# Kernel tuning notes

Measured on AMD Instinct MI355X. Metric: run time of the kernel, lower is better.

## Reference

```python
import jax, jax.numpy as jnp
import numpy as np

MAX_CLUSTERS = 5
CLUSTER_SIZE_MAX = 3
K_HOP = 2
TAU = 1.0  # epoch=0 -> tau_init * decay^0 = 1.0
NEG = -1e9


def _logits(x, ctx, W1, b1, W2, b2):
    # x: [B,N,D], ctx: [B,H] -> logits [B,N] (selection_mlp, dropout=eval/identity)
    B, N, _ = x.shape
    h = jnp.concatenate([x, jnp.broadcast_to(ctx[:, None, :], (B, N, ctx.shape[-1]))], axis=-1)
    h = jax.nn.relu(h @ W1.T + b1)
    return (h @ W2.T + b2)[..., 0]


def _select(logits, cand, key):
    # Hard Gumbel-Softmax argmax over candidate nodes; zeros row if no candidates.
    any_c = cand.any(axis=-1, keepdims=True)
    ml = jnp.where(cand, logits, NEG)
    u = jax.random.uniform(key, logits.shape, dtype=logits.dtype)
    g = -jnp.log(-jnp.log(u + 1e-8) + 1e-8)
    idx = jnp.argmax((ml + g) / TAU, axis=-1)
    oh = jax.nn.one_hot(idx, logits.shape[-1], dtype=logits.dtype)
    return oh * any_c.astype(logits.dtype)


def _gru(seq, h0, Wih, Whh, bih, bhh):
    # torch nn.GRU single layer, batch_first; seq: [B,T,D], h0: [B,H] -> final hidden [B,H]
    def cell(h, xt):
        gi = xt @ Wih.T + bih
        gh = h @ Whh.T + bhh
        ir, iz, inn = jnp.split(gi, 3, axis=-1)
        hr, hz, hn = jnp.split(gh, 3, axis=-1)
        r = jax.nn.sigmoid(ir + hr)
        z = jax.nn.sigmoid(iz + hz)
        n = jnp.tanh(inn + r * hn)
        return (1.0 - z) * n + z * h, None
    h, _ = jax.lax.scan(cell, h0, jnp.swapaxes(seq, 0, 1))
    return h


def reference(x, adj, mask, W1, b1, W2, b2, Wc, bc, Wih, Whh, bih, bhh):
    B, N, D = x.shape
    key = jax.random.key(42)
    avail = mask.astype(bool)
    ctx = x.mean(axis=1) @ Wc.T + bc          # context_init  [B,H]
    h_gru = jnp.zeros_like(ctx)               # context_hidden
    assign = jnp.zeros((B, N, MAX_CLUSTERS), x.dtype)
    embs, hist = [], []
    for c in range(MAX_CLUSTERS):
        # logits are identical for every selection within this cluster (same x, same context)
        logits = _logits(x, ctx, W1, b1, W2, b2)  # [B,N]
        # seed selection (torch uses .item() -> selection is a constant index; no grad path)
        seed = jax.lax.stop_gradient(_select(logits, avail, jax.random.fold_in(key, 2 * c)))
        avail = avail & ~(seed > 0.5)
        # k-hop BFS from seed via adjacency matvecs
        reach = seed > 0.5
        cur = seed
        for _ in range(K_HOP):
            nb = jnp.einsum('bn,bnm->bm', cur, adj) > 0
            new = nb & ~reach
            reach = reach | nb
            cur = new.astype(x.dtype)
        member = seed
        for a in range(CLUSTER_SIZE_MAX - 1):
            cand = avail & reach
            sel = jax.lax.stop_gradient(_select(logits, cand, jax.random.fold_in(key, 2 * c + 1000 + a)))
            avail = avail & ~(sel > 0.5)
            member = member + sel
        assign = assign.at[:, :, c].set(member)
        cnt = member.sum(axis=-1, keepdims=True)
        emb = jnp.einsum('bn,bnd->bd', member, x) / jnp.maximum(cnt, 1.0)  # mean of member feats; 0 if empty
        embs.append(emb)
        hist.append(emb)
        # torch re-runs the GRU over the FULL cluster history each iteration, starting
        # from the previously updated hidden state (faithful to the original code)
        h_gru = _gru(jnp.stack(hist, axis=1), h_gru, Wih, Whh, bih, bhh)
        ctx = h_gru
    cluster_features = jnp.stack(embs, axis=1)               # [B,S,D]
    S = MAX_CLUSTERS
    cluster_adj = jnp.ones((B, S, S), x.dtype) - jnp.eye(S, dtype=x.dtype)[None]
    return cluster_features, cluster_adj, assign


def setup_inputs() -> dict:
    key = jax.random.key(0)
    ks = jax.random.split(key, 10)
    B, N, D, H = 16, 2048, 128, 64
    x = jax.random.normal(ks[0], (B, N, D), dtype=jnp.float32)
    # sparse symmetric binary adjacency, ~16 neighbors per node
    a = (jax.random.uniform(ks[1], (B, N, N)) < 0.004).astype(jnp.float32)
    adj = jnp.clip(a + jnp.swapaxes(a, 1, 2), 0.0, 1.0)
    adj = adj * (1.0 - jnp.eye(N, dtype=jnp.float32)[None])
    mask = jnp.ones((B, N), dtype=jnp.int32)
    s = 0.05
    return {
        'x': x, 'adj': adj, 'mask': mask,
        'W1': jax.random.normal(ks[2], (H, D + H)) * s, 'b1': jnp.zeros((H,)),
        'W2': jax.random.normal(ks[3], (1, H)) * s, 'b2': jnp.zeros((1,)),
        'Wc': jax.random.normal(ks[4], (H, D)) * s, 'bc': jnp.zeros((H,)),
        'Wih': jax.random.normal(ks[5], (3 * H, D)) * s,
        'Whh': jax.random.normal(ks[6], (3 * H, H)) * s,
        'bih': jnp.zeros((3 * H,)), 'bhh': jnp.zeros((3 * H,)),
    }
```

## Files before the change

kernel.cpp:

```cpp
#include <hip/hip_runtime.h>
#include <cfloat>
#include <cmath>

#define NB 2048
#define BB 16
#define DD 128
#define HH 64
#define MAXC 5
#define CSMAX 3
#define NT 1024

__device__ __forceinline__ unsigned rotl32(unsigned v, int d) {
  return (v << d) | (v >> (32 - d));
}

__device__ __forceinline__ void tf2x32(unsigned k0, unsigned k1, unsigned x0, unsigned x1,
                                       unsigned& o0, unsigned& o1) {
  unsigned ks2 = k0 ^ k1 ^ 0x1BD11BDAu;
  x0 += k0; x1 += k1;
#define RND(r) { x0 += x1; x1 = rotl32(x1, r); x1 ^= x0; }
  RND(13) RND(15) RND(26) RND(6)   x0 += k1;  x1 += ks2 + 1u;
  RND(17) RND(29) RND(16) RND(24)  x0 += ks2; x1 += k0 + 2u;
  RND(13) RND(15) RND(26) RND(6)   x0 += k0;  x1 += k1 + 3u;
  RND(17) RND(29) RND(16) RND(24)  x0 += k1;  x1 += ks2 + 4u;
  RND(13) RND(15) RND(26) RND(6)   x0 += ks2; x1 += k0 + 5u;
#undef RND
  o0 = x0; o1 = x1;
}

__device__ __forceinline__ float gumbel_for(unsigned k0, unsigned k1, unsigned idx) {
  unsigned o0, o1;
  tf2x32(k0, k1, 0u, idx, o0, o1);
  unsigned bits = o0 ^ o1;
  float u = __uint_as_float((bits >> 9) | 0x3f800000u) - 1.0f;
  float uu = u + 1e-8f;
  return -logf(-logf(uu) + 1e-8f);
}

__global__ __launch_bounds__(NT) void gvp_prep(
    const float* __restrict__ x, const float* __restrict__ W1,
    float* __restrict__ P, float* __restrict__ partial, float* __restrict__ gumb) {
  __shared__ __align__(16) float s_W1[HH][DD + 4];
  __shared__ float sp[8][DD];
  const int bid = blockIdx.x, tid = threadIdx.x;

  if (bid < 128) {
    for (int i = tid; i < HH * (DD / 4); i += NT) {
      int r = i >> 5, q = i & 31;
      *(float4*)&s_W1[r][q * 4] = *(const float4*)(W1 + (size_t)r * (DD + HH) + q * 4);
    }
    __syncthreads();
    const int jg = tid & 15, ng = tid >> 4;
    const int j0 = jg * 4;
    const size_t n0 = (size_t)bid * 256 + ng * 4;
    const float4* x4 = (const float4*)x;
    float acc[4][4];
#pragma unroll
    for (int i = 0; i < 4; i++)
#pragma unroll
      for (int q = 0; q < 4; q++) acc[i][q] = 0.f;
    for (int kq = 0; kq < 32; kq++) {
      float4 xv[4], wv[4];
#pragma unroll
      for (int i = 0; i < 4; i++) xv[i] = x4[(n0 + i) * 32 + kq];
#pragma unroll
      for (int q = 0; q < 4; q++) wv[q] = *(const float4*)&s_W1[j0 + q][kq * 4];
#pragma unroll
      for (int i = 0; i < 4; i++)
#pragma unroll
        for (int q = 0; q < 4; q++)
          acc[i][q] += xv[i].x * wv[q].x + xv[i].y * wv[q].y +
                       xv[i].z * wv[q].z + xv[i].w * wv[q].w;
    }
#pragma unroll
    for (int i = 0; i < 4; i++)
#pragma unroll
      for (int q = 0; q < 4; q++)
        P[(n0 + i) * HH + j0 + q] = acc[i][q];
  } else if (bid < 384) {
    const int bm = bid - 128;
    const int b = bm >> 4, chunk = bm & 15;
    const int d = tid & (DD - 1), part = tid >> 7;
    float acc = 0.f;
    const int base = chunk * 128 + part;
#pragma unroll
    for (int k = 0; k < 16; k++)
      acc += x[((size_t)b * NB + base + k * 8) * DD + d];
    sp[part][d] = acc;
    __syncthreads();
    if (tid < DD) {
      float m = 0.f;
#pragma unroll
      for (int p = 0; p < 8; p++) m += sp[p][tid];
      partial[((size_t)b * 16 + chunk) * DD + tid] = m;
    }
  } else {
    const int bg = bid - 384;
    const int base = (bg * NT + tid) * 4;
#pragma unroll
    for (int i = 0; i < 4; i++) {
      int idx = base + i;
      int sel = idx >> 15;
      int rem = idx & 32767;
      int c = sel / 3, s = sel - 3 * c;
      unsigned data = (s == 0) ? (unsigned)(2 * c) : (unsigned)(2 * c + 1000 + (s - 1));
      unsigned k0, k1;
      tf2x32(0u, 42u, 0u, data, k0, k1);
      gumb[idx] = gumbel_for(k0, k1, (unsigned)rem);
    }
  }
}

__global__ __launch_bounds__(NT) void gvp_main(
    const float* __restrict__ x, const float* __restrict__ adj, const int* __restrict__ mask,
    const float* __restrict__ W1, const float* __restrict__ b1,
    const float* __restrict__ W2, const float* __restrict__ b2,
    const float* __restrict__ Wc, const float* __restrict__ bc,
    const float* __restrict__ Wih, const float* __restrict__ Whh,
    const float* __restrict__ bih, const float* __restrict__ bhh,
    const float* __restrict__ P, const float* __restrict__ partial,
    const float* __restrict__ gumb,
    float* __restrict__ out_feat, float* __restrict__ out_adjm, float* __restrict__ out_assign) {
  const int b = blockIdx.x;
  const int tid = threadIdx.x;
  const int wid = tid >> 6;

  __shared__ __align__(16) float s_logits[NB];
  __shared__ __align__(16) float s_gumb[2][NB];
  __shared__ unsigned char s_avail[NB], s_reach[NB];
  __shared__ short s_list[128];
  __shared__ int s_cnt;
  __shared__ __align__(16) float s_ctx[HH], s_q[HH], s_h[HH];
  __shared__ __align__(16) float s_hist[MAXC][DD];
  __shared__ __align__(16) float s_giAll[MAXC][3 * HH];
  __shared__ float s_gh[3 * HH];
  __shared__ __align__(16) float s_Whh[3 * HH][HH + 4];
  __shared__ __align__(16) float s_W1c[HH][HH + 4];
  __shared__ __align__(16) float s_W2[HH];
  __shared__ float s_bhh[3 * HH], s_b1[HH];
  __shared__ __align__(16) float s_mean[DD];
  __shared__ __align__(16) float s_emb[CSMAX][DD];
  __shared__ float s_redv[16];
  __shared__ int s_redi[16];
  __shared__ int s_mem[CSMAX];
  __shared__ int s_memCnt, s_selIdx;
  __shared__ float s_b2v;

  const size_t xb = (size_t)b * NB * DD;
  const float4* adj4 = (const float4*)(adj + (size_t)b * NB * NB);
  const float4* P4 = (const float4*)(P + (size_t)b * NB * HH);

  auto finalReduce = [&]() {
    if (tid < 16) {
      float bv = s_redv[tid];
      int bi = s_redi[tid];
#pragma unroll
      for (int off = 8; off; off >>= 1) {
        float ov = __shfl_down(bv, off);
        int oi = __shfl_down(bi, off);
        if (ov > bv || (ov == bv && oi < bi)) { bv = ov; bi = oi; }
      }
      if (tid == 0) {
        int sidx = (bv > -FLT_MAX) ? bi : -1;
        s_selIdx = sidx;
        s_cnt = 0;
        if (sidx >= 0) { s_avail[sidx] = 0; s_mem[s_memCnt++] = sidx; }
      }
    }
  };

  for (int i = tid; i < 3 * HH * (HH / 4); i += NT) {
    int r = i >> 4, q = i & 15;
    *(float4*)&s_Whh[r][q * 4] = *(const float4*)(Whh + (size_t)r * HH + q * 4);
  }
  {
    int r = tid >> 4, q = tid & 15;
    *(float4*)&s_W1c[r][q * 4] = *(const float4*)(W1 + (size_t)r * (DD + HH) + DD + q * 4);
  }
  if (tid < 3 * HH) s_bhh[tid] = bhh[tid];
  if (tid < HH) { s_W2[tid] = W2[tid]; s_b1[tid] = b1[tid]; s_h[tid] = 0.f; }
  if (tid == 0) { s_b2v = b2[0]; s_memCnt = 0; }
#pragma unroll
  for (int r = 0; r < 2; r++) {
    int n = tid + r * NT;
    s_avail[n] = (mask[b * NB + n] != 0) ? 1 : 0;
  }
  if (tid < DD) {
    float m = 0.f;
#pragma unroll
    for (int k = 0; k < 16; k++) m += partial[((size_t)b * 16 + k) * DD + tid];
    s_mean[tid] = m * (1.0f / NB);
  }
  __syncthreads();
  if (tid < 4 * HH) {
    int row = tid >> 2, g = tid & 3;
    const float4* wr = (const float4*)(Wc + (size_t)row * DD) + g * 8;
    const float4* m4 = (const float4*)s_mean + g * 8;
    float s = 0.f;
#pragma unroll
    for (int i = 0; i < 8; i++) {
      float4 w = wr[i], m = m4[i];
      s += w.x * m.x + w.y * m.y + w.z * m.z + w.w * m.w;
    }
    s += __shfl_xor(s, 1);
    s += __shfl_xor(s, 2);
    if (g == 0) s_ctx[row] = s + bc[row];
  }
  __syncthreads();

  for (int c = 0; c < MAXC; c++) {
    const float* g0p = gumb + ((size_t)(c * 3) * BB + b) * NB;
    const float4* g12 = (const float4*)(gumb + ((size_t)(c * 3 + 1 + (tid >> 9)) * BB + b) * NB);
    float4 gst = g12[tid & 511];
    const int n0 = tid, n1 = tid + NT;
    float gs0 = g0p[n0], gs1 = g0p[n1];
    if (tid < 4 * HH) {
      int row = tid >> 2, g = tid & 3;
      const float4* wr = (const float4*)&s_W1c[row][0] + g * 4;
      const float4* c4 = (const float4*)s_ctx + g * 4;
      float s = 0.f;
#pragma unroll
      for (int i = 0; i < 4; i++) {
        float4 w = wr[i], cc = c4[i];
        s += w.x * cc.x + w.y * cc.y + w.z * cc.z + w.w * cc.w;
      }
      s += __shfl_xor(s, 1);
      s += __shfl_xor(s, 2);
      if (g == 0) s_q[row] = s + s_b1[row];
    }
    if (tid == 0) s_memCnt = 0;
    __syncthreads();

    {
      float l0 = s_b2v, l1 = s_b2v;
      const float4* p0 = P4 + (size_t)n0 * 16;
      const float4* p1 = P4 + (size_t)n1 * 16;
      const float4* q4 = (const float4*)s_q;
      const float4* w4 = (const float4*)s_W2;
#pragma unroll
      for (int q = 0; q < 16; q++) {
        float4 pa = p0[q], pb = p1[q], qq = q4[q], w = w4[q];
        l0 += w.x * fmaxf(pa.x + qq.x, 0.f) + w.y * fmaxf(pa.y + qq.y, 0.f) +
              w.z * fmaxf(pa.z + qq.z, 0.f) + w.w * fmaxf(pa.w + qq.w, 0.f);
        l1 += w.x * fmaxf(pb.x + qq.x, 0.f) + w.y * fmaxf(pb.y + qq.y, 0.f) +
              w.z * fmaxf(pb.z + qq.z, 0.f) + w.w * fmaxf(pb.w + qq.w, 0.f);
      }
      s_logits[n0] = l0;
      s_logits[n1] = l1;
      float bestv = -FLT_MAX;
      int besti = NB;
      if (s_avail[n0]) { float y = l0 + gs0; if (y > bestv) { bestv = y; besti = n0; } }
      if (s_avail[n1]) { float y = l1 + gs1; if (y > bestv) { bestv = y; besti = n1; } }
#pragma unroll
      for (int off = 32; off; off >>= 1) {
        float ov = __shfl_down(bestv, off);
        int oi = __shfl_down(besti, off);
        if (ov > bestv || (ov == bestv && oi < besti)) { bestv = ov; besti = oi; }
      }
      if ((tid & 63) == 0) { s_redv[wid] = bestv; s_redi[wid] = besti; }
      ((float4*)s_gumb)[tid] = gst;
    }
    __syncthreads();
    finalReduce();
    __syncthreads();
    const int seed = s_selIdx;

    if (tid < 512) {
      if (seed >= 0) {
        float4 a = adj4[(size_t)seed * 512 + tid];
        int m = tid << 2;
        unsigned f0 = a.x > 0.f, f1 = a.y > 0.f, f2 = a.z > 0.f, f3 = a.w > 0.f;
        unsigned r = f0 | (f1 << 8) | (f2 << 16) | (f3 << 24);
        if ((seed >> 2) == tid) r |= 1u << ((seed & 3) * 8);
        ((unsigned*)s_reach)[tid] = r;
        if (f0 && m != seed)     { int p = atomicAdd(&s_cnt, 1); if (p < 128) s_list[p] = (short)m; }
        if (f1 && m + 1 != seed) { int p = atomicAdd(&s_cnt, 1); if (p < 128) s_list[p] = (short)(m + 1); }
        if (f2 && m + 2 != seed) { int p = atomicAdd(&s_cnt, 1); if (p < 128) s_list[p] = (short)(m + 2); }
        if (f3 && m + 3 != seed) { int p = atomicAdd(&s_cnt, 1); if (p < 128) s_list[p] = (short)(m + 3); }
      } else {
        ((unsigned*)s_reach)[tid] = 0u;
      }
    }
    __syncthreads();

    if (seed >= 0) {
      int cnt = min(s_cnt, 128);
      int m4 = tid & 511, rg = tid >> 9;
      bool a0 = false, a1 = false, a2 = false, a3 = false;
#pragma unroll
      for (int k = 0; k < 20; k++) {
        int li = rg + 2 * k;
        if (li < cnt) {
          int n = s_list[li];
          float4 a = adj4[(size_t)n * 512 + m4];
          a0 |= a.x > 0.f; a1 |= a.y > 0.f; a2 |= a.z > 0.f; a3 |= a.w > 0.f;
        }
      }
      for (int li = rg + 40; li < cnt; li += 2) {
        int n = s_list[li];
        float4 a = adj4[(size_t)n * 512 + m4];
        a0 |= a.x > 0.f; a1 |= a.y > 0.f; a2 |= a.z > 0.f; a3 |= a.w > 0.f;
      }
      int m = m4 << 2;
      if (a0) s_reach[m] = 1;
      if (a1) s_reach[m + 1] = 1;
      if (a2) s_reach[m + 2] = 1;
      if (a3) s_reach[m + 3] = 1;
    }
    __syncthreads();

    for (int s = 1; s < CSMAX; s++) {
      float bv = -FLT_MAX;
      int bi = NB;
#pragma unroll
      for (int r = 0; r < 2; r++) {
        int n = tid + r * NT;
        if (s_avail[n] && s_reach[n]) {
          float y = s_logits[n] + s_gumb[s - 1][n];
          if (y > bv) { bv = y; bi = n; }
        }
      }
#pragma unroll
      for (int off = 32; off; off >>= 1) {
        float ov = __shfl_down(bv, off);
        int oi = __shfl_down(bi, off);
        if (ov > bv || (ov == bv && oi < bi)) { bv = ov; bi = oi; }
      }
      if ((tid & 63) == 0) { s_redv[wid] = bv; s_redi[wid] = bi; }
      __syncthreads();
      finalReduce();
      __syncthreads();
    }

    {
      int mc = s_memCnt;
      int mm0 = mc > 0 ? s_mem[0] : -1;
      int mm1 = mc > 1 ? s_mem[1] : -1;
      int mm2 = mc > 2 ? s_mem[2] : -1;
#pragma unroll
      for (int r = 0; r < 2; r++) {
        int n = tid + r * NT;
        out_assign[(size_t)(b * NB + n) * MAXC + c] =
            (n == mm0 || n == mm1 || n == mm2) ? 1.0f : 0.0f;
      }
      if (tid < 384) {
        int rr = tid >> 7, d = tid & (DD - 1);
        if (rr < mc) s_emb[rr][d] = x[xb + (size_t)s_mem[rr] * DD + d];
      }
    }
    __syncthreads();
    if (tid < DD) {
      int mc = s_memCnt;
      float acc = 0.f;
      if (mc > 0) acc += s_emb[0][tid];
      if (mc > 1) acc += s_emb[1][tid];
      if (mc > 2) acc += s_emb[2][tid];
      float e = acc / fmaxf((float)mc, 1.0f);
      s_hist[c][tid] = e;
      out_feat[((size_t)b * MAXC + c) * DD + tid] = e;
    }
    __syncthreads();

    if (tid < 4 * 3 * HH) {
      int row = tid >> 2, g = tid & 3;
      const float4* wr = (const float4*)(Wih + (size_t)row * DD) + g * 8;
      const float4* h4 = (const float4*)s_hist[c] + g * 8;
      float s = 0.f;
#pragma unroll
      for (int i = 0; i < 8; i++) {
        float4 w = wr[i], hh = h4[i];
        s += w.x * hh.x + w.y * hh.y + w.z * hh.z + w.w * hh.w;
      }
      s += __shfl_xor(s, 1);
      s += __shfl_xor(s, 2);
      if (g == 0) s_giAll[c][row] = s + bih[row];
    }
    __syncthreads();

    for (int t0 = 0; t0 <= c; t0++) {
      if (tid < 4 * 3 * HH) {
        int row = tid >> 2, g = tid & 3;
        const float4* wr = (const float4*)&s_Whh[row][0] + g * 4;
        const float4* h4 = (const float4*)s_h + g * 4;
        float s = 0.f;
#pragma unroll
        for (int i = 0; i < 4; i++) {
          float4 w = wr[i], hh = h4[i];
          s += w.x * hh.x + w.y * hh.y + w.z * hh.z + w.w * hh.w;
        }
        s += __shfl_xor(s, 1);
        s += __shfl_xor(s, 2);
        if (g == 0) s_gh[row] = s + s_bhh[row];
      }
      __syncthreads();
      if (tid < HH) {
        float r = 1.f / (1.f + expf(-(s_giAll[t0][tid] + s_gh[tid])));
        float z = 1.f / (1.f + expf(-(s_giAll[t0][HH + tid] + s_gh[HH + tid])));
        float nn = tanhf(s_giAll[t0][2 * HH + tid] + r * s_gh[2 * HH + tid]);
        float hn = (1.f - z) * nn + z * s_h[tid];
        s_h[tid] = hn;
        if (t0 == c) s_ctx[tid] = hn;
      }
      __syncthreads();
    }
  }

  for (int i = tid; i < MAXC * MAXC; i += NT)
    out_adjm[(size_t)b * MAXC * MAXC + i] = ((i / MAXC) == (i % MAXC)) ? 0.f : 1.f;
}

extern "C" void kernel_launch(void* const* d_in, const int* in_sizes, int n_in,
                              void* d_out, int out_size, void* d_ws, size_t ws_size,
                              hipStream_t stream) {
  const float* x   = (const float*)d_in[0];
  const float* adj = (const float*)d_in[1];
  const int*   mask= (const int*)d_in[2];
  const float* W1  = (const float*)d_in[3];
  const float* b1  = (const float*)d_in[4];
  const float* W2  = (const float*)d_in[5];
  const float* b2  = (const float*)d_in[6];
  const float* Wc  = (const float*)d_in[7];
  const float* bc  = (const float*)d_in[8];
  const float* Wih = (const float*)d_in[9];
  const float* Whh = (const float*)d_in[10];
  const float* bih = (const float*)d_in[11];
  const float* bhh = (const float*)d_in[12];

  float* ws = (float*)d_ws;
  float* P       = ws;
  float* partial = P + (size_t)BB * NB * HH;
  float* gumb    = partial + (size_t)BB * 16 * DD;

  float* out = (float*)d_out;
  float* out_feat = out;
  float* out_adjm = out + (size_t)BB * MAXC * DD;
  float* out_assign = out_adjm + (size_t)BB * MAXC * MAXC;

  hipLaunchKernelGGL(gvp_prep, dim3(504), dim3(NT), 0, stream, x, W1, P, partial, gumb);
  hipLaunchKernelGGL(gvp_main, dim3(BB), dim3(NT), 0, stream,
                     x, adj, mask, W1, b1, W2, b2, Wc, bc, Wih, Whh, bih, bhh, P, partial, gumb,
                     out_feat, out_adjm, out_assign);
}
```

Measured before the change: 198.6 us.

## Cut block barriers with atomic argmax keys, fused GRU gates, deferred assign writes

```diff
diff --git a/kernel.cpp b/kernel.cpp
--- a/kernel.cpp
+++ b/kernel.cpp
@@ -111,7 +111,7 @@
   }
 }
 
-__global__ __launch_bounds__(NT) void gvp_main(
+__global__ __launch_bounds__(NT, 4) void gvp_main(
     const float* __restrict__ x, const float* __restrict__ adj, const int* __restrict__ mask,
     const float* __restrict__ W1, const float* __restrict__ b1,
     const float* __restrict__ W2, const float* __restrict__ b2,
@@ -123,50 +123,44 @@
     float* __restrict__ out_feat, float* __restrict__ out_adjm, float* __restrict__ out_assign) {
   const int b = blockIdx.x;
   const int tid = threadIdx.x;
-  const int wid = tid >> 6;
 
   __shared__ __align__(16) float s_logits[NB];
   __shared__ __align__(16) float s_gumb[2][NB];
-  __shared__ unsigned char s_avail[NB], s_reach[NB];
+  __shared__ unsigned char s_avail[NB], s_reach[NB], s_assignB[NB];
   __shared__ short s_list[128];
   __shared__ int s_cnt;
-  __shared__ __align__(16) float s_ctx[HH], s_q[HH], s_h[HH];
+  __shared__ unsigned long long s_key[CSMAX];
+  __shared__ __align__(16) float s_ctx[HH], s_q[HH];
+  __shared__ __align__(16) float s_h[2][HH];
   __shared__ __align__(16) float s_hist[MAXC][DD];
   __shared__ __align__(16) float s_giAll[MAXC][3 * HH];
-  __shared__ float s_gh[3 * HH];
   __shared__ __align__(16) float s_Whh[3 * HH][HH + 4];
   __shared__ __align__(16) float s_W1c[HH][HH + 4];
   __shared__ __align__(16) float s_W2[HH];
   __shared__ float s_bhh[3 * HH], s_b1[HH];
   __shared__ __align__(16) float s_mean[DD];
-  __shared__ __align__(16) float s_emb[CSMAX][DD];
-  __shared__ float s_redv[16];
-  __shared__ int s_redi[16];
-  __shared__ int s_mem[CSMAX];
-  __shared__ int s_memCnt, s_selIdx;
   __shared__ float s_b2v;
 
   const size_t xb = (size_t)b * NB * DD;
   const float4* adj4 = (const float4*)(adj + (size_t)b * NB * NB);
   const float4* P4 = (const float4*)(P + (size_t)b * NB * HH);
 
-  auto finalReduce = [&]() {
-    if (tid < 16) {
-      float bv = s_redv[tid];
-      int bi = s_redi[tid];
-#pragma unroll
-      for (int off = 8; off; off >>= 1) {
-        float ov = __shfl_down(bv, off);
-        int oi = __shfl_down(bi, off);
-        if (ov > bv || (ov == bv && oi < bi)) { bv = ov; bi = oi; }
-      }
-      if (tid == 0) {
-        int sidx = (bv > -FLT_MAX) ? bi : -1;
-        s_selIdx = sidx;
-        s_cnt = 0;
-        if (sidx >= 0) { s_avail[sidx] = 0; s_mem[s_memCnt++] = sidx; }
-      }
-    }
+  auto scanReduce = [&](float bv, int bi, int slot) {
+#pragma unroll
+    for (int off = 32; off; off >>= 1) {
+      float ov = __shfl_down(bv, off);
+      int oi = __shfl_down(bi, off);
+      if (ov > bv || (ov == bv && oi < bi)) { bv = ov; bi = oi; }
+    }
+    if ((tid & 63) == 0 && bi < NB) {
+      unsigned u = __float_as_uint(bv);
+      u = (u & 0x80000000u) ? ~u : (u | 0x80000000u);
+      unsigned long long key = ((unsigned long long)u << 32) | (unsigned)(~bi);
+      atomicMax(&s_key[slot], key);
+    }
+  };
+  auto decodeIdx = [](unsigned long long k) -> int {
+    return k ? (int)(unsigned)(~(unsigned)k) : -1;
   };
 
   for (int i = tid; i < 3 * HH * (HH / 4); i += NT) {
@@ -178,12 +172,13 @@
     *(float4*)&s_W1c[r][q * 4] = *(const float4*)(W1 + (size_t)r * (DD + HH) + DD + q * 4);
   }
   if (tid < 3 * HH) s_bhh[tid] = bhh[tid];
-  if (tid < HH) { s_W2[tid] = W2[tid]; s_b1[tid] = b1[tid]; s_h[tid] = 0.f; }
-  if (tid == 0) { s_b2v = b2[0]; s_memCnt = 0; }
+  if (tid < HH) { s_W2[tid] = W2[tid]; s_b1[tid] = b1[tid]; s_h[0][tid] = 0.f; }
+  if (tid == 0) s_b2v = b2[0];
 #pragma unroll
   for (int r = 0; r < 2; r++) {
     int n = tid + r * NT;
     s_avail[n] = (mask[b * NB + n] != 0) ? 1 : 0;
+    s_assignB[n] = 0;
   }
   if (tid < DD) {
     float m = 0.f;
@@ -208,12 +203,15 @@
   }
   __syncthreads();
 
+  int hp = 0;
+
   for (int c = 0; c < MAXC; c++) {
     const float* g0p = gumb + ((size_t)(c * 3) * BB + b) * NB;
     const float4* g12 = (const float4*)(gumb + ((size_t)(c * 3 + 1 + (tid >> 9)) * BB + b) * NB);
     float4 gst = g12[tid & 511];
     const int n0 = tid, n1 = tid + NT;
     float gs0 = g0p[n0], gs1 = g0p[n1];
+    ((float4*)s_gumb)[tid] = gst;
     if (tid < 4 * HH) {
       int row = tid >> 2, g = tid & 3;
       const float4* wr = (const float4*)&s_W1c[row][0] + g * 4;
@@ -228,7 +226,8 @@
       s += __shfl_xor(s, 2);
       if (g == 0) s_q[row] = s + s_b1[row];
     }
-    if (tid == 0) s_memCnt = 0;
+    if (tid < CSMAX) s_key[tid] = 0ull;
+    if (tid == 0) s_cnt = 0;
     __syncthreads();
 
     {
@@ -238,33 +237,30 @@
       const float4* q4 = (const float4*)s_q;
       const float4* w4 = (const float4*)s_W2;
 #pragma unroll
-      for (int q = 0; q < 16; q++) {
-        float4 pa = p0[q], pb = p1[q], qq = q4[q], w = w4[q];
-        l0 += w.x * fmaxf(pa.x + qq.x, 0.f) + w.y * fmaxf(pa.y + qq.y, 0.f) +
-              w.z * fmaxf(pa.z + qq.z, 0.f) + w.w * fmaxf(pa.w + qq.w, 0.f);
-        l1 += w.x * fmaxf(pb.x + qq.x, 0.f) + w.y * fmaxf(pb.y + qq.y, 0.f) +
-              w.z * fmaxf(pb.z + qq.z, 0.f) + w.w * fmaxf(pb.w + qq.w, 0.f);
+      for (int qq = 0; qq < 16; qq += 4) {
+        float4 A[4], Bv[4];
+#pragma unroll
+        for (int i = 0; i < 4; i++) { A[i] = p0[qq + i]; Bv[i] = p1[qq + i]; }
+#pragma unroll
+        for (int i = 0; i < 4; i++) {
+          float4 qv = q4[qq + i], w = w4[qq + i];
+          l0 += w.x * fmaxf(A[i].x + qv.x, 0.f) + w.y * fmaxf(A[i].y + qv.y, 0.f) +
+                w.z * fmaxf(A[i].z + qv.z, 0.f) + w.w * fmaxf(A[i].w + qv.w, 0.f);
+          l1 += w.x * fmaxf(Bv[i].x + qv.x, 0.f) + w.y * fmaxf(Bv[i].y + qv.y, 0.f) +
+                w.z * fmaxf(Bv[i].z + qv.z, 0.f) + w.w * fmaxf(Bv[i].w + qv.w, 0.f);
+        }
       }
       s_logits[n0] = l0;
       s_logits[n1] = l1;
-      float bestv = -FLT_MAX;
-      int besti = NB;
-      if (s_avail[n0]) { float y = l0 + gs0; if (y > bestv) { bestv = y; besti = n0; } }
-      if (s_avail[n1]) { float y = l1 + gs1; if (y > bestv) { bestv = y; besti = n1; } }
-#pragma unroll
-      for (int off = 32; off; off >>= 1) {
-        float ov = __shfl_down(bestv, off);
-        int oi = __shfl_down(besti, off);
-        if (ov > bestv || (ov == bestv && oi < besti)) { bestv = ov; besti = oi; }
-      }
-      if ((tid & 63) == 0) { s_redv[wid] = bestv; s_redi[wid] = besti; }
-      ((float4*)s_gumb)[tid] = gst;
-    }
-    __syncthreads();
-    finalReduce();
-    __syncthreads();
-    const int seed = s_selIdx;
-
+      float bv = -FLT_MAX;
+      int bi = NB;
+      if (s_avail[n0]) { float y = l0 + gs0; if (y > bv) { bv = y; bi = n0; } }
+      if (s_avail[n1]) { float y = l1 + gs1; if (y > bv || (y == bv && n1 < bi)) { bv = y; bi = n1; } }
+      scanReduce(bv, bi, 0);
+    }
+    __syncthreads();
+
+    const int seed = decodeIdx(s_key[0]);
     if (tid < 512) {
       if (seed >= 0) {
         float4 a = adj4[(size_t)seed * 512 + tid];
@@ -309,55 +305,52 @@
     }
     __syncthreads();
 
-    for (int s = 1; s < CSMAX; s++) {
+    {
       float bv = -FLT_MAX;
       int bi = NB;
 #pragma unroll
       for (int r = 0; r < 2; r++) {
         int n = tid + r * NT;
-        if (s_avail[n] && s_reach[n]) {
-          float y = s_logits[n] + s_gumb[s - 1][n];
-          if (y > bv) { bv = y; bi = n; }
-        }
-      }
-#pragma unroll
-      for (int off = 32; off; off >>= 1) {
-        float ov = __shfl_down(bv, off);
-        int oi = __shfl_down(bi, off);
-        if (ov > bv || (ov == bv && oi < bi)) { bv = ov; bi = oi; }
-      }
-      if ((tid & 63) == 0) { s_redv[wid] = bv; s_redi[wid] = bi; }
-      __syncthreads();
-      finalReduce();
-      __syncthreads();
-    }
-
+        if (s_avail[n] && s_reach[n] && n != seed) {
+          float y = s_logits[n] + s_gumb[0][n];
+          if (y > bv || (y == bv && n < bi)) { bv = y; bi = n; }
+        }
+      }
+      scanReduce(bv, bi, 1);
+    }
+    __syncthreads();
+
+    const int w1i = decodeIdx(s_key[1]);
     {
-      int mc = s_memCnt;
-      int mm0 = mc > 0 ? s_mem[0] : -1;
-      int mm1 = mc > 1 ? s_mem[1] : -1;
-      int mm2 = mc > 2 ? s_mem[2] : -1;
+      float bv = -FLT_MAX;
+      int bi = NB;
 #pragma unroll
       for (int r = 0; r < 2; r++) {
         int n = tid + r * NT;
-        out_assign[(size_t)(b * NB + n) * MAXC + c] =
-            (n == mm0 || n == mm1 || n == mm2) ? 1.0f : 0.0f;
-      }
-      if (tid < 384) {
-        int rr = tid >> 7, d = tid & (DD - 1);
-        if (rr < mc) s_emb[rr][d] = x[xb + (size_t)s_mem[rr] * DD + d];
-      }
-    }
-    __syncthreads();
-    if (tid < DD) {
-      int mc = s_memCnt;
-      float acc = 0.f;
-      if (mc > 0) acc += s_emb[0][tid];
-      if (mc > 1) acc += s_emb[1][tid];
-      if (mc > 2) acc += s_emb[2][tid];
-      float e = acc / fmaxf((float)mc, 1.0f);
-      s_hist[c][tid] = e;
-      out_feat[((size_t)b * MAXC + c) * DD + tid] = e;
+        if (s_avail[n] && s_reach[n] && n != seed && n != w1i) {
+          float y = s_logits[n] + s_gumb[1][n];
+          if (y > bv || (y == bv && n < bi)) { bv = y; bi = n; }
+        }
+      }
+      scanReduce(bv, bi, 2);
+    }
+    __syncthreads();
+
+    const int w2i = decodeIdx(s_key[2]);
+    {
+      int mc = (seed >= 0) + (w1i >= 0) + (w2i >= 0);
+      if (tid < DD) {
+        float acc = 0.f;
+        if (seed >= 0) acc += x[xb + (size_t)seed * DD + tid];
+        if (w1i >= 0) acc += x[xb + (size_t)w1i * DD + tid];
+        if (w2i >= 0) acc += x[xb + (size_t)w2i * DD + tid];
+        float e = acc / fmaxf((float)mc, 1.0f);
+        s_hist[c][tid] = e;
+        out_feat[((size_t)b * MAXC + c) * DD + tid] = e;
+      } else if (tid >= 128 && tid < 128 + CSMAX) {
+        int idx = (tid == 128) ? seed : (tid == 129 ? w1i : w2i);
+        if (idx >= 0) { s_avail[idx] = 0; s_assignB[idx] |= (unsigned char)(1 << c); }
+      }
     }
     __syncthreads();
 
@@ -378,33 +371,49 @@
     __syncthreads();
 
     for (int t0 = 0; t0 <= c; t0++) {
-      if (tid < 4 * 3 * HH) {
+      if (tid < 4 * HH) {
         int row = tid >> 2, g = tid & 3;
+        const float4* h4 = (const float4*)s_h[hp] + g * 4;
+        float4 hv[4];
+#pragma unroll
+        for (int i = 0; i < 4; i++) hv[i] = h4[i];
         const float4* wr = (const float4*)&s_Whh[row][0] + g * 4;
-        const float4* h4 = (const float4*)s_h + g * 4;
-        float s = 0.f;
+        const float4* wz = (const float4*)&s_Whh[HH + row][0] + g * 4;
+        const float4* wn = (const float4*)&s_Whh[2 * HH + row][0] + g * 4;
+        float sr = 0.f, sz = 0.f, sn = 0.f;
 #pragma unroll
         for (int i = 0; i < 4; i++) {
-          float4 w = wr[i], hh = h4[i];
-          s += w.x * hh.x + w.y * hh.y + w.z * hh.z + w.w * hh.w;
-        }
-        s += __shfl_xor(s, 1);
-        s += __shfl_xor(s, 2);
-        if (g == 0) s_gh[row] = s + s_bhh[row];
-      }
+          float4 a = wr[i], bz = wz[i], cn = wn[i], h = hv[i];
+          sr += a.x * h.x + a.y * h.y + a.z * h.z + a.w * h.w;
+          sz += bz.x * h.x + bz.y * h.y + bz.z * h.z + bz.w * h.w;
+          sn += cn.x * h.x + cn.y * h.y + cn.z * h.z + cn.w * h.w;
+        }
+        sr += __shfl_xor(sr, 1); sr += __shfl_xor(sr, 2);
+        sz += __shfl_xor(sz, 1); sz += __shfl_xor(sz, 2);
+        sn += __shfl_xor(sn, 1); sn += __shfl_xor(sn, 2);
+        if (g == 0) {
+          float r = 1.f / (1.f + expf(-(s_giAll[t0][row] + sr + s_bhh[row])));
+          float z = 1.f / (1.f + expf(-(s_giAll[t0][HH + row] + sz + s_bhh[HH + row])));
+          float nn = tanhf(s_giAll[t0][2 * HH + row] + r * (sn + s_bhh[2 * HH + row]));
+          float hn = (1.f - z) * nn + z * s_h[hp][row];
+          s_h[hp ^ 1][row] = hn;
+          if (t0 == c) s_ctx[row] = hn;
+        }
+      }
+      hp ^= 1;
       __syncthreads();
-      if (tid < HH) {
-        float r = 1.f / (1.f + expf(-(s_giAll[t0][tid] + s_gh[tid])));
-        float z = 1.f / (1.f + expf(-(s_giAll[t0][HH + tid] + s_gh[HH + tid])));
-        float nn = tanhf(s_giAll[t0][2 * HH + tid] + r * s_gh[2 * HH + tid]);
-        float hn = (1.f - z) * nn + z * s_h[tid];
-        s_h[tid] = hn;
-        if (t0 == c) s_ctx[tid] = hn;
-      }
-      __syncthreads();
-    }
-  }
-
+    }
+  }
+
+#pragma unroll
+  for (int r = 0; r < 2; r++) {
+    int n = tid + r * NT;
+    unsigned bits = s_assignB[n];
+    size_t base = ((size_t)(b * NB + n)) * MAXC;
+#pragma unroll
+    for (int cc = 0; cc < MAXC; cc++)
+      out_assign[base + cc] = (float)((bits >> cc) & 1u);
+  }
   for (int i = tid; i < MAXC * MAXC; i += NT)
     out_adjm[(size_t)b * MAXC * MAXC + i] = ((i / MAXC) == (i % MAXC)) ? 0.f : 1.f;
 }
```

Result: no change. 195.0 us (-1.9%).
